# Optimization experiments

Hardware: AMD Instinct MI355X
Metric: run time of the kernel (lower is better)

## Reference

```python
import jax, jax.numpy as jnp
import numpy as np

T = 8388608  # sequence length (2^23)
WIDTH = 1.0


def phi(x, width=WIDTH):
    # Phi(x) = x if x > 0; x + width if x < -width; 0 otherwise
    return jnp.maximum(x, 0.0) + jnp.minimum(x + width, 0.0)


def setup_inputs() -> dict:
    key = jax.random.key(0)
    k1, k2 = jax.random.split(key)
    inputs = jax.random.normal(k1, (1, T), dtype=jnp.float32)
    state = jnp.zeros((1, 1), dtype=jnp.float32)
    # non_neg constrained scalar weight
    kernel = jax.random.uniform(k2, (1, 1), dtype=jnp.float32)
    return {"inputs": inputs, "state": state, "kernel": kernel}


def reference(inputs, state, kernel):
    # outputs_ = inputs * kernel (scalar multiply), then sequential hysteresis scan:
    #   out_i = Phi(outputs_[i] - out_{i-1}) + out_{i-1}
    xs = (inputs * kernel[0, 0])[0]  # [T]

    def step(prev, x):
        out = phi(x - prev) + prev
        return out, out

    last, outs = jax.lax.scan(step, state[0, 0], xs)
    outputs = outs.reshape(inputs.shape)       # [1, T]
    new_state = last.reshape(1, 1)             # [1, 1]
    return outputs, new_state
```

## Files before the change

kernel.cpp:

```cpp
#include <hip/hip_runtime.h>
#include <math.h>


#define TPB 256
#define WAVES (TPB / 64)
#define SEGS 4
#define FPL 8
#define SEG_ELEMS (TPB * FPL)
#define ELEMS (SEGS * SEG_ELEMS)

__device__ __forceinline__ float clampf(float x, float lo, float hi) {
    return fminf(fmaxf(x, lo), hi);
}

__global__ __launch_bounds__(TPB) void k_agg(const float4* __restrict__ x4,
                                             const float* __restrict__ kern,
                                             float2* __restrict__ agg) {
    __shared__ float wl[SEGS][WAVES], wh[SEGS][WAVES];
    const int t = threadIdx.x, lane = t & 63, w = t >> 6;
    const int b = blockIdx.x;
    const float k = kern[0];
    const size_t base4 = (size_t)b * (ELEMS / 4);

#pragma unroll
    for (int s = 0; s < SEGS; ++s) {
        const size_t i4 = base4 + (size_t)s * (SEG_ELEMS / 4) + (size_t)t * 2;
        float4 v0 = x4[i4], v1 = x4[i4 + 1];
        float lo, hi, a;
        a = v0.x * k; lo = a; hi = a + 1.0f;
        a = v0.y * k; lo = clampf(lo, a, a + 1.0f); hi = clampf(hi, a, a + 1.0f);
        a = v0.z * k; lo = clampf(lo, a, a + 1.0f); hi = clampf(hi, a, a + 1.0f);
        a = v0.w * k; lo = clampf(lo, a, a + 1.0f); hi = clampf(hi, a, a + 1.0f);
        a = v1.x * k; lo = clampf(lo, a, a + 1.0f); hi = clampf(hi, a, a + 1.0f);
        a = v1.y * k; lo = clampf(lo, a, a + 1.0f); hi = clampf(hi, a, a + 1.0f);
        a = v1.z * k; lo = clampf(lo, a, a + 1.0f); hi = clampf(hi, a, a + 1.0f);
        a = v1.w * k; lo = clampf(lo, a, a + 1.0f); hi = clampf(hi, a, a + 1.0f);
#pragma unroll
        for (int off = 1; off < 64; off <<= 1) {
            float plo = __shfl_down(lo, off);
            float phi_ = __shfl_down(hi, off);
            float nlo = clampf(lo, plo, phi_);
            float nhi = clampf(hi, plo, phi_);
            lo = nlo; hi = nhi;
        }
        if (lane == 0) { wl[s][w] = lo; wh[s][w] = hi; }
    }
    __syncthreads();
    if (t == 0) {
        float L = -INFINITY, H = INFINITY;
#pragma unroll
        for (int s = 0; s < SEGS; ++s)
#pragma unroll
            for (int i = 0; i < WAVES; ++i) {
                L = clampf(L, wl[s][i], wh[s][i]);
                H = clampf(H, wl[s][i], wh[s][i]);
            }
        agg[b] = make_float2(L, H);
    }
}

__global__ __launch_bounds__(TPB) void k_apply(
    const float4* __restrict__ x4,
    const float* __restrict__ kern,
    const float* __restrict__ state,
    const float2* __restrict__ agg,
    float* __restrict__ out,
    int nblocks)
{
    __shared__ float rl[WAVES], rh[WAVES];
    __shared__ float wtl[SEGS][WAVES], wth[SEGS][WAVES];
    __shared__ float s_vb;

    const int t = threadIdx.x, lane = t & 63, w = t >> 6;
    const int b = blockIdx.x;
    const float k = kern[0];
    const size_t base4 = (size_t)b * (ELEMS / 4);

    {
        const int per = nblocks / TPB;
        float lo = -INFINITY, hi = INFINITY;
#pragma unroll
        for (int c = 0; c < per; ++c) {
            int j = t * per + c;
            if (j < b) {
                float2 ag = agg[j];
                lo = clampf(lo, ag.x, ag.y);
                hi = clampf(hi, ag.x, ag.y);
            }
        }
#pragma unroll
        for (int off = 1; off < 64; off <<= 1) {
            float plo = __shfl_down(lo, off);
            float phi_ = __shfl_down(hi, off);
            float nlo = clampf(lo, plo, phi_);
            float nhi = clampf(hi, plo, phi_);
            lo = nlo; hi = nhi;
        }
        if (lane == 0) { rl[w] = lo; rh[w] = hi; }
    }
    __syncthreads();
    if (t == 0) {
        float L = rl[0], H = rh[0];
#pragma unroll
        for (int i = 1; i < WAVES; ++i) {
            L = clampf(L, rl[i], rh[i]);
            H = clampf(H, rl[i], rh[i]);
        }
        s_vb = clampf(state[0], L, H);
    }

    float a[SEGS][FPL];
    float eslo[SEGS], eshi[SEGS];
    float Slo[SEGS], Shi[SEGS];

#pragma unroll
    for (int s = 0; s < SEGS; ++s) {
        const size_t i4 = base4 + (size_t)s * (SEG_ELEMS / 4) + (size_t)t * 2;
        float4 v0 = x4[i4], v1 = x4[i4 + 1];
        a[s][0] = v0.x * k; a[s][1] = v0.y * k; a[s][2] = v0.z * k; a[s][3] = v0.w * k;
        a[s][4] = v1.x * k; a[s][5] = v1.y * k; a[s][6] = v1.z * k; a[s][7] = v1.w * k;
        float lo = a[s][0], hi = a[s][0] + 1.0f;
#pragma unroll
        for (int c = 1; c < FPL; ++c) {
            lo = clampf(lo, a[s][c], a[s][c] + 1.0f);
            hi = clampf(hi, a[s][c], a[s][c] + 1.0f);
        }
#pragma unroll
        for (int off = 1; off < 64; off <<= 1) {
            float plo = __shfl_up(lo, off);
            float phi_ = __shfl_up(hi, off);
            if (lane >= off) {
                float nlo = clampf(plo, lo, hi);
                float nhi = clampf(phi_, lo, hi);
                lo = nlo; hi = nhi;
            }
        }
        float elo = __shfl_up(lo, 1), ehi = __shfl_up(hi, 1);
        if (lane == 0) { elo = -INFINITY; ehi = INFINITY; }
        eslo[s] = elo; eshi[s] = ehi;
        if (lane == 63) { wtl[s][w] = lo; wth[s][w] = hi; }
    }
    __syncthreads();

#pragma unroll
    for (int s = 0; s < SEGS; ++s) {
        float welo = -INFINITY, wehi = INFINITY;
        for (int i = 0; i < w; ++i) {
            welo = clampf(welo, wtl[s][i], wth[s][i]);
            wehi = clampf(wehi, wtl[s][i], wth[s][i]);
        }
        float llo = eslo[s], lhi = eshi[s];
        eslo[s] = clampf(welo, llo, lhi);
        eshi[s] = clampf(wehi, llo, lhi);
        float stl = -INFINITY, sth = INFINITY;
#pragma unroll
        for (int i = 0; i < WAVES; ++i) {
            stl = clampf(stl, wtl[s][i], wth[s][i]);
            sth = clampf(sth, wtl[s][i], wth[s][i]);
        }
        Slo[s] = stl; Shi[s] = sth;
    }

    __syncthreads();
    float p = s_vb;
    float wv = p;
#pragma unroll
    for (int s = 0; s < SEGS; ++s) {
        wv = clampf(p, eslo[s], eshi[s]);
        float4 r0, r1;
        wv = clampf(wv, a[s][0], a[s][0] + 1.0f); r0.x = wv;
        wv = clampf(wv, a[s][1], a[s][1] + 1.0f); r0.y = wv;
        wv = clampf(wv, a[s][2], a[s][2] + 1.0f); r0.z = wv;
        wv = clampf(wv, a[s][3], a[s][3] + 1.0f); r0.w = wv;
        wv = clampf(wv, a[s][4], a[s][4] + 1.0f); r1.x = wv;
        wv = clampf(wv, a[s][5], a[s][5] + 1.0f); r1.y = wv;
        wv = clampf(wv, a[s][6], a[s][6] + 1.0f); r1.z = wv;
        wv = clampf(wv, a[s][7], a[s][7] + 1.0f); r1.w = wv;
        float4* o = (float4*)(out + (size_t)b * ELEMS + (size_t)s * SEG_ELEMS) + (size_t)t * 2;
        o[0] = r0; o[1] = r1;
        p = clampf(p, Slo[s], Shi[s]);
    }

    if (b == nblocks - 1 && t == TPB - 1)
        out[(size_t)nblocks * ELEMS] = wv;
}

extern "C" void kernel_launch(void* const* d_in, const int* in_sizes, int n_in,
                              void* d_out, int out_size, void* d_ws, size_t ws_size,
                              hipStream_t stream) {
    const float4* x4   = (const float4*)d_in[0];
    const float* state = (const float*)d_in[1];
    const float* kern  = (const float*)d_in[2];
    float* out = (float*)d_out;

    const size_t T = (size_t)in_sizes[0];
    const int nblocks = (int)(T / ELEMS);
    float2* agg = (float2*)d_ws;

    k_agg<<<nblocks, TPB, 0, stream>>>(x4, kern, agg);
    k_apply<<<nblocks, TPB, 0, stream>>>(x4, kern, state, agg, out, nblocks);
}
```

Baseline: 99.29 us.

## Fuse aggregate and apply passes into one cooperative kernel with grid sync

Combines the two-pass scan into one cooperative kernel. Each block loads its input tile once, keeps it in registers, publishes its block aggregate with an atomic release store, and waits at a grid-wide barrier. It then combines earlier blocks' aggregates and writes the outputs. This removes the second full read of the input and one kernel launch, at the cost of a grid barrier. It also requires all 1024 blocks to be co-resident, which is why launch bounds ask for 4 blocks per CU. If the cooperative launch fails, it falls back to the original two kernels.

```diff
diff --git a/kernel.cpp b/kernel.cpp
--- a/kernel.cpp
+++ b/kernel.cpp
@@ -1,5 +1,8 @@
 #include <hip/hip_runtime.h>
+#include <hip/hip_cooperative_groups.h>
 #include <math.h>
+
+namespace cg = cooperative_groups;
 
 
 #define TPB 256
@@ -13,101 +16,22 @@
     return fminf(fmaxf(x, lo), hi);
 }
 
-__global__ __launch_bounds__(TPB) void k_agg(const float4* __restrict__ x4,
-                                             const float* __restrict__ kern,
-                                             float2* __restrict__ agg) {
-    __shared__ float wl[SEGS][WAVES], wh[SEGS][WAVES];
+__global__ __launch_bounds__(TPB, 4) void k_fused(
+    const float4* __restrict__ x4,
+    const float* __restrict__ kern,
+    const float* __restrict__ state,
+    unsigned long long* __restrict__ agg,
+    float* __restrict__ out,
+    int nblocks)
+{
+    __shared__ float wtl[SEGS][WAVES], wth[SEGS][WAVES];
+    __shared__ float rl[WAVES], rh[WAVES];
+    __shared__ float s_vb;
+
     const int t = threadIdx.x, lane = t & 63, w = t >> 6;
     const int b = blockIdx.x;
     const float k = kern[0];
     const size_t base4 = (size_t)b * (ELEMS / 4);
-
-#pragma unroll
-    for (int s = 0; s < SEGS; ++s) {
-        const size_t i4 = base4 + (size_t)s * (SEG_ELEMS / 4) + (size_t)t * 2;
-        float4 v0 = x4[i4], v1 = x4[i4 + 1];
-        float lo, hi, a;
-        a = v0.x * k; lo = a; hi = a + 1.0f;
-        a = v0.y * k; lo = clampf(lo, a, a + 1.0f); hi = clampf(hi, a, a + 1.0f);
-        a = v0.z * k; lo = clampf(lo, a, a + 1.0f); hi = clampf(hi, a, a + 1.0f);
-        a = v0.w * k; lo = clampf(lo, a, a + 1.0f); hi = clampf(hi, a, a + 1.0f);
-        a = v1.x * k; lo = clampf(lo, a, a + 1.0f); hi = clampf(hi, a, a + 1.0f);
-        a = v1.y * k; lo = clampf(lo, a, a + 1.0f); hi = clampf(hi, a, a + 1.0f);
-        a = v1.z * k; lo = clampf(lo, a, a + 1.0f); hi = clampf(hi, a, a + 1.0f);
-        a = v1.w * k; lo = clampf(lo, a, a + 1.0f); hi = clampf(hi, a, a + 1.0f);
-#pragma unroll
-        for (int off = 1; off < 64; off <<= 1) {
-            float plo = __shfl_down(lo, off);
-            float phi_ = __shfl_down(hi, off);
-            float nlo = clampf(lo, plo, phi_);
-            float nhi = clampf(hi, plo, phi_);
-            lo = nlo; hi = nhi;
-        }
-        if (lane == 0) { wl[s][w] = lo; wh[s][w] = hi; }
-    }
-    __syncthreads();
-    if (t == 0) {
-        float L = -INFINITY, H = INFINITY;
-#pragma unroll
-        for (int s = 0; s < SEGS; ++s)
-#pragma unroll
-            for (int i = 0; i < WAVES; ++i) {
-                L = clampf(L, wl[s][i], wh[s][i]);
-                H = clampf(H, wl[s][i], wh[s][i]);
-            }
-        agg[b] = make_float2(L, H);
-    }
-}
-
-__global__ __launch_bounds__(TPB) void k_apply(
-    const float4* __restrict__ x4,
-    const float* __restrict__ kern,
-    const float* __restrict__ state,
-    const float2* __restrict__ agg,
-    float* __restrict__ out,
-    int nblocks)
-{
-    __shared__ float rl[WAVES], rh[WAVES];
-    __shared__ float wtl[SEGS][WAVES], wth[SEGS][WAVES];
-    __shared__ float s_vb;
-
-    const int t = threadIdx.x, lane = t & 63, w = t >> 6;
-    const int b = blockIdx.x;
-    const float k = kern[0];
-    const size_t base4 = (size_t)b * (ELEMS / 4);
-
-    {
-        const int per = nblocks / TPB;
-        float lo = -INFINITY, hi = INFINITY;
-#pragma unroll
-        for (int c = 0; c < per; ++c) {
-            int j = t * per + c;
-            if (j < b) {
-                float2 ag = agg[j];
-                lo = clampf(lo, ag.x, ag.y);
-                hi = clampf(hi, ag.x, ag.y);
-            }
-        }
-#pragma unroll
-        for (int off = 1; off < 64; off <<= 1) {
-            float plo = __shfl_down(lo, off);
-            float phi_ = __shfl_down(hi, off);
-            float nlo = clampf(lo, plo, phi_);
-            float nhi = clampf(hi, plo, phi_);
-            lo = nlo; hi = nhi;
-        }
-        if (lane == 0) { rl[w] = lo; rh[w] = hi; }
-    }
-    __syncthreads();
-    if (t == 0) {
-        float L = rl[0], H = rh[0];
-#pragma unroll
-        for (int i = 1; i < WAVES; ++i) {
-            L = clampf(L, rl[i], rh[i]);
-            H = clampf(H, rl[i], rh[i]);
-        }
-        s_vb = clampf(state[0], L, H);
-    }
 
     float a[SEGS][FPL];
     float eslo[SEGS], eshi[SEGS];
@@ -161,7 +85,57 @@
         Slo[s] = stl; Shi[s] = sth;
     }
 
-    __syncthreads();
+    if (t == 0) {
+        float L = -INFINITY, H = INFINITY;
+#pragma unroll
+        for (int s = 0; s < SEGS; ++s) {
+            L = clampf(L, Slo[s], Shi[s]);
+            H = clampf(H, Slo[s], Shi[s]);
+        }
+        float2 p2 = make_float2(L, H);
+        unsigned long long u;
+        __builtin_memcpy(&u, &p2, 8);
+        __hip_atomic_store(&agg[b], u, __ATOMIC_RELEASE, __HIP_MEMORY_SCOPE_AGENT);
+    }
+
+    cg::this_grid().sync();
+
+    {
+        const int per = nblocks / TPB;
+        float lo = -INFINITY, hi = INFINITY;
+#pragma unroll
+        for (int c = 0; c < 4; ++c) {
+            int j = t * per + c;
+            if (c < per && j < b) {
+                unsigned long long u =
+                    __hip_atomic_load(&agg[j], __ATOMIC_RELAXED, __HIP_MEMORY_SCOPE_AGENT);
+                float2 ag; __builtin_memcpy(&ag, &u, 8);
+                lo = clampf(lo, ag.x, ag.y);
+                hi = clampf(hi, ag.x, ag.y);
+            }
+        }
+#pragma unroll
+        for (int off = 1; off < 64; off <<= 1) {
+            float plo = __shfl_down(lo, off);
+            float phi_ = __shfl_down(hi, off);
+            float nlo = clampf(lo, plo, phi_);
+            float nhi = clampf(hi, plo, phi_);
+            lo = nlo; hi = nhi;
+        }
+        if (lane == 0) { rl[w] = lo; rh[w] = hi; }
+    }
+    __syncthreads();
+    if (t == 0) {
+        float L = rl[0], H = rh[0];
+#pragma unroll
+        for (int i = 1; i < WAVES; ++i) {
+            L = clampf(L, rl[i], rh[i]);
+            H = clampf(H, rl[i], rh[i]);
+        }
+        s_vb = clampf(state[0], L, H);
+    }
+    __syncthreads();
+
     float p = s_vb;
     float wv = p;
 #pragma unroll
@@ -185,6 +159,178 @@
         out[(size_t)nblocks * ELEMS] = wv;
 }
 
+__global__ __launch_bounds__(TPB) void k_agg(const float4* __restrict__ x4,
+                                             const float* __restrict__ kern,
+                                             float2* __restrict__ agg) {
+    __shared__ float wl[SEGS][WAVES], wh[SEGS][WAVES];
+    const int t = threadIdx.x, lane = t & 63, w = t >> 6;
+    const int b = blockIdx.x;
+    const float k = kern[0];
+    const size_t base4 = (size_t)b * (ELEMS / 4);
+
+#pragma unroll
+    for (int s = 0; s < SEGS; ++s) {
+        const size_t i4 = base4 + (size_t)s * (SEG_ELEMS / 4) + (size_t)t * 2;
+        float4 v0 = x4[i4], v1 = x4[i4 + 1];
+        float lo, hi, a;
+        a = v0.x * k; lo = a; hi = a + 1.0f;
+        a = v0.y * k; lo = clampf(lo, a, a + 1.0f); hi = clampf(hi, a, a + 1.0f);
+        a = v0.z * k; lo = clampf(lo, a, a + 1.0f); hi = clampf(hi, a, a + 1.0f);
+        a = v0.w * k; lo = clampf(lo, a, a + 1.0f); hi = clampf(hi, a, a + 1.0f);
+        a = v1.x * k; lo = clampf(lo, a, a + 1.0f); hi = clampf(hi, a, a + 1.0f);
+        a = v1.y * k; lo = clampf(lo, a, a + 1.0f); hi = clampf(hi, a, a + 1.0f);
+        a = v1.z * k; lo = clampf(lo, a, a + 1.0f); hi = clampf(hi, a, a + 1.0f);
+        a = v1.w * k; lo = clampf(lo, a, a + 1.0f); hi = clampf(hi, a, a + 1.0f);
+#pragma unroll
+        for (int off = 1; off < 64; off <<= 1) {
+            float plo = __shfl_down(lo, off);
+            float phi_ = __shfl_down(hi, off);
+            float nlo = clampf(lo, plo, phi_);
+            float nhi = clampf(hi, plo, phi_);
+            lo = nlo; hi = nhi;
+        }
+        if (lane == 0) { wl[s][w] = lo; wh[s][w] = hi; }
+    }
+    __syncthreads();
+    if (t == 0) {
+        float L = -INFINITY, H = INFINITY;
+#pragma unroll
+        for (int s = 0; s < SEGS; ++s)
+#pragma unroll
+            for (int i = 0; i < WAVES; ++i) {
+                L = clampf(L, wl[s][i], wh[s][i]);
+                H = clampf(H, wl[s][i], wh[s][i]);
+            }
+        agg[b] = make_float2(L, H);
+    }
+}
+
+__global__ __launch_bounds__(TPB) void k_apply(
+    const float4* __restrict__ x4,
+    const float* __restrict__ kern,
+    const float* __restrict__ state,
+    const float2* __restrict__ agg,
+    float* __restrict__ out,
+    int nblocks)
+{
+    __shared__ float rl[WAVES], rh[WAVES];
+    __shared__ float wtl[SEGS][WAVES], wth[SEGS][WAVES];
+    __shared__ float s_vb;
+
+    const int t = threadIdx.x, lane = t & 63, w = t >> 6;
+    const int b = blockIdx.x;
+    const float k = kern[0];
+    const size_t base4 = (size_t)b * (ELEMS / 4);
+
+    {
+        const int per = nblocks / TPB;
+        float lo = -INFINITY, hi = INFINITY;
+#pragma unroll
+        for (int c = 0; c < 4; ++c) {
+            int j = t * per + c;
+            if (c < per && j < b) {
+                float2 ag = agg[j];
+                lo = clampf(lo, ag.x, ag.y);
+                hi = clampf(hi, ag.x, ag.y);
+            }
+        }
+#pragma unroll
+        for (int off = 1; off < 64; off <<= 1) {
+            float plo = __shfl_down(lo, off);
+            float phi_ = __shfl_down(hi, off);
+            float nlo = clampf(lo, plo, phi_);
+            float nhi = clampf(hi, plo, phi_);
+            lo = nlo; hi = nhi;
+        }
+        if (lane == 0) { rl[w] = lo; rh[w] = hi; }
+    }
+    __syncthreads();
+    if (t == 0) {
+        float L = rl[0], H = rh[0];
+#pragma unroll
+        for (int i = 1; i < WAVES; ++i) {
+            L = clampf(L, rl[i], rh[i]);
+            H = clampf(H, rl[i], rh[i]);
+        }
+        s_vb = clampf(state[0], L, H);
+    }
+
+    float a[SEGS][FPL];
+    float eslo[SEGS], eshi[SEGS];
+    float Slo[SEGS], Shi[SEGS];
+
+#pragma unroll
+    for (int s = 0; s < SEGS; ++s) {
+        const size_t i4 = base4 + (size_t)s * (SEG_ELEMS / 4) + (size_t)t * 2;
+        float4 v0 = x4[i4], v1 = x4[i4 + 1];
+        a[s][0] = v0.x * k; a[s][1] = v0.y * k; a[s][2] = v0.z * k; a[s][3] = v0.w * k;
+        a[s][4] = v1.x * k; a[s][5] = v1.y * k; a[s][6] = v1.z * k; a[s][7] = v1.w * k;
+        float lo = a[s][0], hi = a[s][0] + 1.0f;
+#pragma unroll
+        for (int c = 1; c < FPL; ++c) {
+            lo = clampf(lo, a[s][c], a[s][c] + 1.0f);
+            hi = clampf(hi, a[s][c], a[s][c] + 1.0f);
+        }
+#pragma unroll
+        for (int off = 1; off < 64; off <<= 1) {
+            float plo = __shfl_up(lo, off);
+            float phi_ = __shfl_up(hi, off);
+            if (lane >= off) {
+                float nlo = clampf(plo, lo, hi);
+                float nhi = clampf(phi_, lo, hi);
+                lo = nlo; hi = nhi;
+            }
+        }
+        float elo = __shfl_up(lo, 1), ehi = __shfl_up(hi, 1);
+        if (lane == 0) { elo = -INFINITY; ehi = INFINITY; }
+        eslo[s] = elo; eshi[s] = ehi;
+        if (lane == 63) { wtl[s][w] = lo; wth[s][w] = hi; }
+    }
+    __syncthreads();
+
+#pragma unroll
+    for (int s = 0; s < SEGS; ++s) {
+        float welo = -INFINITY, wehi = INFINITY;
+        for (int i = 0; i < w; ++i) {
+            welo = clampf(welo, wtl[s][i], wth[s][i]);
+            wehi = clampf(wehi, wtl[s][i], wth[s][i]);
+        }
+        float llo = eslo[s], lhi = eshi[s];
+        eslo[s] = clampf(welo, llo, lhi);
+        eshi[s] = clampf(wehi, llo, lhi);
+        float stl = -INFINITY, sth = INFINITY;
+#pragma unroll
+        for (int i = 0; i < WAVES; ++i) {
+            stl = clampf(stl, wtl[s][i], wth[s][i]);
+            sth = clampf(sth, wtl[s][i], wth[s][i]);
+        }
+        Slo[s] = stl; Shi[s] = sth;
+    }
+
+    __syncthreads();
+    float p = s_vb;
+    float wv = p;
+#pragma unroll
+    for (int s = 0; s < SEGS; ++s) {
+        wv = clampf(p, eslo[s], eshi[s]);
+        float4 r0, r1;
+        wv = clampf(wv, a[s][0], a[s][0] + 1.0f); r0.x = wv;
+        wv = clampf(wv, a[s][1], a[s][1] + 1.0f); r0.y = wv;
+        wv = clampf(wv, a[s][2], a[s][2] + 1.0f); r0.z = wv;
+        wv = clampf(wv, a[s][3], a[s][3] + 1.0f); r0.w = wv;
+        wv = clampf(wv, a[s][4], a[s][4] + 1.0f); r1.x = wv;
+        wv = clampf(wv, a[s][5], a[s][5] + 1.0f); r1.y = wv;
+        wv = clampf(wv, a[s][6], a[s][6] + 1.0f); r1.z = wv;
+        wv = clampf(wv, a[s][7], a[s][7] + 1.0f); r1.w = wv;
+        float4* o = (float4*)(out + (size_t)b * ELEMS + (size_t)s * SEG_ELEMS) + (size_t)t * 2;
+        o[0] = r0; o[1] = r1;
+        p = clampf(p, Slo[s], Shi[s]);
+    }
+
+    if (b == nblocks - 1 && t == TPB - 1)
+        out[(size_t)nblocks * ELEMS] = wv;
+}
+
 extern "C" void kernel_launch(void* const* d_in, const int* in_sizes, int n_in,
                               void* d_out, int out_size, void* d_ws, size_t ws_size,
                               hipStream_t stream) {
@@ -194,9 +340,18 @@
     float* out = (float*)d_out;
 
     const size_t T = (size_t)in_sizes[0];
-    const int nblocks = (int)(T / ELEMS);
-    float2* agg = (float2*)d_ws;
-
-    k_agg<<<nblocks, TPB, 0, stream>>>(x4, kern, agg);
-    k_apply<<<nblocks, TPB, 0, stream>>>(x4, kern, state, agg, out, nblocks);
-}
+    int nblocks = (int)(T / ELEMS);
+
+    unsigned long long* agg_u = (unsigned long long*)d_ws;
+
+    void* args[] = { (void*)&x4, (void*)&kern, (void*)&state,
+                     (void*)&agg_u, (void*)&out, (void*)&nblocks };
+    hipError_t err = hipLaunchCooperativeKernel(
+        (const void*)k_fused, dim3(nblocks), dim3(TPB), args, 0, stream);
+
+    if (err != hipSuccess) {
+        float2* agg = (float2*)d_ws;
+        k_agg<<<nblocks, TPB, 0, stream>>>(x4, kern, agg);
+        k_apply<<<nblocks, TPB, 0, stream>>>(x4, kern, state, agg, out, nblocks);
+    }
+}
```

After: 225.1 us. +126.7%, slower.
